# Optimization experiments

Hardware: AMD Instinct MI355X
Metric: run time of the kernel (lower is better)

The kernel has to match this reference:

```python
import jax, jax.numpy as jnp
import numpy as np

D = 768          # hidden_size
M = 8            # num_patchmerges
B = 16
S = 2048         # non-CLF tokens


def setup_inputs() -> dict:
    key = jax.random.key(0)
    ks = jax.random.split(key, 12)
    std = 0.02
    tokens = jax.random.normal(ks[0], (B, 1 + S, D), dtype=jnp.float32)
    lengths = jnp.maximum(jax.random.randint(ks[1], (B,), 0, S), 1).astype(jnp.int64)
    # PatchMerger: learned queries + layernorm params
    q = jax.random.normal(ks[2], (M, D), dtype=jnp.float32) * std
    ln_scale = jnp.ones((D,), dtype=jnp.float32)
    ln_bias = jnp.zeros((D,), dtype=jnp.float32)
    # mlp1: Linear(3D, D) -> GELU -> Linear(D, D)
    w1a = jax.random.normal(ks[3], (3 * D, D), dtype=jnp.float32) * std
    b1a = jnp.zeros((D,), dtype=jnp.float32)
    w2a = jax.random.normal(ks[4], (D, D), dtype=jnp.float32) * std
    b2a = jnp.zeros((D,), dtype=jnp.float32)
    # mlp2: Linear((1+M)D, D) -> GELU -> Linear(D, D)
    w1b = jax.random.normal(ks[5], ((1 + M) * D, D), dtype=jnp.float32) * std
    b1b = jnp.zeros((D,), dtype=jnp.float32)
    w2b = jax.random.normal(ks[6], (D, D), dtype=jnp.float32) * std
    b2b = jnp.zeros((D,), dtype=jnp.float32)
    return dict(tokens=tokens, lengths=lengths, q=q, ln_scale=ln_scale,
                ln_bias=ln_bias, w1a=w1a, b1a=b1a, w2a=w2a, b2a=b2a,
                w1b=w1b, b1b=b1b, w2b=w2b, b2b=b2b)


def _hpmlp(x, w1, b1, w2, b2):
    h = jax.nn.gelu(x @ w1 + b1, approximate=False)  # dropout=0 -> identity
    return h @ w2 + b2


def _layernorm(x, scale, bias, eps=1e-5):
    mu = jnp.mean(x, axis=-1, keepdims=True)
    var = jnp.var(x, axis=-1, keepdims=True)
    return (x - mu) * jax.lax.rsqrt(var + eps) * scale + bias


def reference(tokens, lengths, q, ln_scale, ln_bias,
              w1a, b1a, w2a, b2a, w1b, b1b, w2b, b2b):
    clf = tokens[:, 0]            # [B, D]
    x = tokens[:, 1:]             # [B, S, D]
    mask = jnp.arange(S)[None, :] < lengths[:, None]   # [B, S]
    mf = mask[..., None].astype(x.dtype)

    # fixed path: masked mean / max / min over valid tokens
    denom = lengths.astype(x.dtype)[:, None]
    mean_p = jnp.sum(x * mf, axis=1) / denom
    max_p = jnp.max(jnp.where(mask[..., None], x, -jnp.inf), axis=1)
    min_p = jnp.min(jnp.where(mask[..., None], x, jnp.inf), axis=1)
    pooled_trad = jnp.concatenate([mean_p, max_p, min_p], axis=-1)  # [B, 3D]
    out_fixed = _hpmlp(pooled_trad, w1a, b1a, w2a, b2a)

    # learned path: PatchMerger (masked attention from M learned queries)
    xn = _layernorm(x, ln_scale, ln_bias)
    scores = jnp.einsum('md,bsd->bms', q, xn) / jnp.sqrt(jnp.asarray(D, x.dtype))
    scores = jnp.where(mask[:, None, :], scores, -jnp.inf)
    attn = jax.nn.softmax(scores, axis=-1)                # [B, M, S]
    merged = jnp.einsum('bms,bsd->bmd', attn, x)          # [B, M, D]
    pooled_learn = jnp.concatenate([merged.reshape(B, M * D), clf], axis=-1)
    out_learn = _hpmlp(pooled_learn, w1b, b1b, w2b, b2b)

    return jnp.concatenate([out_fixed, out_learn], axis=-1)  # [B, 2D]
```

## Files before the change

### kernel.cpp

```cpp
#include <hip/hip_runtime.h>
#include <math.h>

#define SD 768
#define SB 16
#define SM 8
#define SS 2048
#define TOK_ROW 2049
#define NEG_INF (-__builtin_inff())

#define OFF_PPOOL   0
#define OFF_PO      2359296
#define OFF_PML     8650752
#define OFF_PTRAD   8667136
#define OFF_PLEARN  8704000
#define OFF_P1A     8814592
#define OFF_P1B     9035776
#define OFF_HA      9699328
#define OFF_HB      9711616
#define OFF_P2A     9723904
#define OFF_P2B     9797632

__device__ __forceinline__ int clen(int v) { return v < 1 ? 1 : (v > SS ? SS : v); }

__global__ __launch_bounds__(256, 2) void k1_flash(
    const float* __restrict__ tokens, const int* __restrict__ lengths,
    const float* __restrict__ q, const float* __restrict__ lns,
    const float* __restrict__ lnb, float* __restrict__ ppool,
    float* __restrict__ pO, float* __restrict__ pml) {
  int c = blockIdx.x, b = blockIdx.y;
  int len = clen(lengths[b]);
  int c0 = c * 32;
  if (c0 >= len) return;
  int tid = threadIdx.x, w = tid >> 6, lane = tid & 63;
  int mm = lane & 7;

  __shared__ float p_lds[4][8][8];
  __shared__ float pool_lds[4][3][SD];
  __shared__ float O_lds[SM][SD];
  __shared__ float l_lds[4][8];

  if (tid < 256) { (&p_lds[0][0][0])[tid] = 0.f; }

  float4 qr[8][3];
  float qs1sel, qbsel;
  {
    float4 l4[3], lb4[3];
    #pragma unroll
    for (int g = 0; g < 3; ++g) {
      l4[g] = *(const float4*)(lns + g * 256 + lane * 4);
      lb4[g] = *(const float4*)(lnb + g * 256 + lane * 4);
    }
    float qs1r[8], qbr[8];
    #pragma unroll
    for (int m = 0; m < 8; ++m) {
      float s1 = 0.f, sb = 0.f;
      #pragma unroll
      for (int g = 0; g < 3; ++g) {
        float4 qv = *(const float4*)(q + m * SD + g * 256 + lane * 4);
        float4 qs;
        qs.x = qv.x * l4[g].x; qs.y = qv.y * l4[g].y;
        qs.z = qv.z * l4[g].z; qs.w = qv.w * l4[g].w;
        qr[m][g] = qs;
        s1 += qs.x + qs.y + qs.z + qs.w;
        sb += qv.x * lb4[g].x + qv.y * lb4[g].y + qv.z * lb4[g].z + qv.w * lb4[g].w;
      }
      #pragma unroll
      for (int o = 32; o; o >>= 1) { s1 += __shfl_xor(s1, o, 64); sb += __shfl_xor(sb, o, 64); }
      qs1r[m] = s1; qbr[m] = sb;
    }
    qs1sel = qs1r[0]; qbsel = qbr[0];
    #pragma unroll
    for (int m = 1; m < 8; ++m) {
      qs1sel = (mm == m) ? qs1r[m] : qs1sel;
      qbsel = (mm == m) ? qbr[m] : qbsel;
    }
  }
  __syncthreads();

  float psum[12], pmax[12], pmin[12];
  #pragma unroll
  for (int j = 0; j < 12; ++j) { psum[j] = 0.f; pmax[j] = NEG_INF; pmin[j] = -NEG_INF; }

  int srow = c0 + w * 8;
  int smax = len - srow; if (smax > 8) smax = 8; if (smax < 0) smax = 0;
  const float* xrow = tokens + ((size_t)b * TOK_ROW + 1 + srow) * SD;
  float l_run = 0.f;

  float4 nx0 = {}, nx1 = {}, nx2 = {};
  if (smax > 0) {
    nx0 = *(const float4*)(xrow + lane * 4);
    nx1 = *(const float4*)(xrow + 256 + lane * 4);
    nx2 = *(const float4*)(xrow + 512 + lane * 4);
  }
  for (int i = 0; i < smax; ++i) {
    float4 x0 = nx0, x1 = nx1, x2 = nx2;
    if (i + 1 < smax) {
      const float* xq = xrow + (size_t)(i + 1) * SD;
      nx0 = *(const float4*)(xq + lane * 4);
      nx1 = *(const float4*)(xq + 256 + lane * 4);
      nx2 = *(const float4*)(xq + 512 + lane * 4);
    }
    float xv[12] = {x0.x, x0.y, x0.z, x0.w, x1.x, x1.y, x1.z, x1.w,
                    x2.x, x2.y, x2.z, x2.w};
    float s1 = 0.f, s2 = 0.f;
    #pragma unroll
    for (int j = 0; j < 12; ++j) {
      float v = xv[j];
      psum[j] += v;
      pmax[j] = fmaxf(pmax[j], v);
      pmin[j] = fminf(pmin[j], v);
      s1 += v;
      s2 += v * v;
    }
    float d[8];
    #pragma unroll
    for (int m = 0; m < 8; ++m) {
      float4 a0 = qr[m][0], a1 = qr[m][1], a2 = qr[m][2];
      d[m] = a0.x * xv[0] + a0.y * xv[1] + a0.z * xv[2] + a0.w * xv[3]
           + a1.x * xv[4] + a1.y * xv[5] + a1.z * xv[6] + a1.w * xv[7]
           + a2.x * xv[8] + a2.y * xv[9] + a2.z * xv[10] + a2.w * xv[11];
    }
    #pragma unroll
    for (int o = 1; o <= 4; o <<= 1)
      #pragma unroll
      for (int m = 0; m < 8; ++m) d[m] += __shfl_xor(d[m], o, 64);
    float u = d[0];
    #pragma unroll
    for (int m = 1; m < 8; ++m) u = (mm == m) ? d[m] : u;
    #pragma unroll
    for (int o = 8; o <= 32; o <<= 1) {
      u += __shfl_xor(u, o, 64);
      s1 += __shfl_xor(s1, o, 64);
      s2 += __shfl_xor(s2, o, 64);
    }
    #pragma unroll
    for (int o = 1; o <= 4; o <<= 1) { s1 += __shfl_xor(s1, o, 64); s2 += __shfl_xor(s2, o, 64); }
    float mu = s1 * (1.f / 768.f);
    float var = s2 * (1.f / 768.f) - mu * mu;
    float rstd = rsqrtf(var + 1e-5f);
    float sc = (rstd * u - rstd * mu * qs1sel + qbsel) * 0.03608439182435161f;
    float pe = __expf(sc);
    l_run += pe;
    if (lane < 8) p_lds[w][i][lane] = pe;
  }

  #pragma unroll
  for (int g = 0; g < 3; ++g) {
    int dd = g * 256 + lane * 4;
    *(float4*)&pool_lds[w][0][dd] = make_float4(psum[g*4], psum[g*4+1], psum[g*4+2], psum[g*4+3]);
    *(float4*)&pool_lds[w][1][dd] = make_float4(pmax[g*4], pmax[g*4+1], pmax[g*4+2], pmax[g*4+3]);
    *(float4*)&pool_lds[w][2][dd] = make_float4(pmin[g*4], pmin[g*4+1], pmin[g*4+2], pmin[g*4+3]);
  }
  if (lane < 8) l_lds[w][lane] = l_run;
  __syncthreads();

  if (tid < 8) {
    size_t base = (size_t)(c * SB + b) * 16;
    pml[base + tid] = 0.f;
    pml[base + 8 + tid] = l_lds[0][tid] + l_lds[1][tid] + l_lds[2][tid] + l_lds[3][tid];
  }

  float O[8][12];
  #pragma unroll
  for (int m = 0; m < 8; ++m)
    #pragma unroll
    for (int j = 0; j < 12; ++j) O[m][j] = 0.f;
  float4 a0v = {}, a1v = {}, a2v = {}, b0v = {}, b1v = {}, b2v = {};
  if (smax > 0) {
    a0v = *(const float4*)(xrow + lane * 4);
    a1v = *(const float4*)(xrow + 256 + lane * 4);
    a2v = *(const float4*)(xrow + 512 + lane * 4);
  }
  if (smax > 1) {
    const float* xq = xrow + SD;
    b0v = *(const float4*)(xq + lane * 4);
    b1v = *(const float4*)(xq + 256 + lane * 4);
    b2v = *(const float4*)(xq + 512 + lane * 4);
  }
  for (int i = 0; i < smax; ++i) {
    float4 x0 = a0v, x1 = a1v, x2 = a2v;
    a0v = b0v; a1v = b1v; a2v = b2v;
    if (i + 2 < smax) {
      const float* xq = xrow + (size_t)(i + 2) * SD;
      b0v = *(const float4*)(xq + lane * 4);
      b1v = *(const float4*)(xq + 256 + lane * 4);
      b2v = *(const float4*)(xq + 512 + lane * 4);
    }
    float xv[12] = {x0.x, x0.y, x0.z, x0.w, x1.x, x1.y, x1.z, x1.w,
                    x2.x, x2.y, x2.z, x2.w};
    const float4* pr = (const float4*)&p_lds[w][i][0];
    float4 pa = pr[0], pb = pr[1];
    float pm[8] = {pa.x, pa.y, pa.z, pa.w, pb.x, pb.y, pb.z, pb.w};
    #pragma unroll
    for (int m = 0; m < 8; ++m)
      #pragma unroll
      for (int j = 0; j < 12; ++j) O[m][j] += pm[m] * xv[j];
  }
  #pragma unroll
  for (int r = 0; r < 4; ++r) {
    if (w == r) {
      #pragma unroll
      for (int m = 0; m < 8; ++m)
        #pragma unroll
        for (int g = 0; g < 3; ++g) {
          int dd = g * 256 + lane * 4;
          float4 mine = make_float4(O[m][g*4], O[m][g*4+1], O[m][g*4+2], O[m][g*4+3]);
          if (r == 0) {
            *(float4*)&O_lds[m][dd] = mine;
          } else {
            float4 cur = *(float4*)&O_lds[m][dd];
            cur.x += mine.x; cur.y += mine.y; cur.z += mine.z; cur.w += mine.w;
            *(float4*)&O_lds[m][dd] = cur;
          }
        }
    }
    __syncthreads();
  }

  size_t obase = (size_t)(c * SB + b) * 6144;
  const float* of = &O_lds[0][0];
  for (int j = tid * 4; j < 6144; j += 1024)
    *(float4*)&pO[obase + j] = *(const float4*)&of[j];

  size_t pbase = (size_t)(c * SB + b) * 2304;
  for (int j4 = tid * 4; j4 < 2304; j4 += 1024) {
    int stat = j4 / SD, dd = j4 - stat * SD;
    float4 v0 = *(float4*)&pool_lds[0][stat][dd];
    float4 v1 = *(float4*)&pool_lds[1][stat][dd];
    float4 v2 = *(float4*)&pool_lds[2][stat][dd];
    float4 v3 = *(float4*)&pool_lds[3][stat][dd];
    float4 r;
    if (stat == 0) {
      r.x = v0.x + v1.x + v2.x + v3.x; r.y = v0.y + v1.y + v2.y + v3.y;
      r.z = v0.z + v1.z + v2.z + v3.z; r.w = v0.w + v1.w + v2.w + v3.w;
    } else if (stat == 1) {
      r.x = fmaxf(fmaxf(v0.x, v1.x), fmaxf(v2.x, v3.x));
      r.y = fmaxf(fmaxf(v0.y, v1.y), fmaxf(v2.y, v3.y));
      r.z = fmaxf(fmaxf(v0.z, v1.z), fmaxf(v2.z, v3.z));
      r.w = fmaxf(fmaxf(v0.w, v1.w), fmaxf(v2.w, v3.w));
    } else {
      r.x = fminf(fminf(v0.x, v1.x), fminf(v2.x, v3.x));
      r.y = fminf(fminf(v0.y, v1.y), fminf(v2.y, v3.y));
      r.z = fminf(fminf(v0.z, v1.z), fminf(v2.z, v3.z));
      r.w = fminf(fminf(v0.w, v1.w), fminf(v2.w, v3.w));
    }
    *(float4*)&ppool[pbase + j4] = r;
  }
}

__global__ void k_combine(const float* __restrict__ ppool, const float* __restrict__ pO,
                          const float* __restrict__ pml, const float* __restrict__ tokens,
                          const int* __restrict__ lengths,
                          float* __restrict__ ptrad, float* __restrict__ plearn) {
  int tile = blockIdx.x, b = blockIdx.y;
  int len = clen(lengths[b]);
  int nv = (len + 31) >> 5;
  int tid = threadIdx.x;
  __shared__ float pml_lds[64][16];
  __shared__ float e_lds[64][8];
  __shared__ float Linv_lds[8];
  for (int t = tid; t < nv * 16; t += 256) {
    int cc = t >> 4, j = t & 15;
    pml_lds[cc][j] = pml[(size_t)(cc * SB + b) * 16 + j];
  }
  __syncthreads();
  if (tid < 8) {
    float M = NEG_INF;
    for (int cc = 0; cc < nv; ++cc) M = fmaxf(M, pml_lds[cc][tid]);
    float L = 0.f;
    for (int cc = 0; cc < nv; ++cc) {
      float e = __expf(pml_lds[cc][tid] - M);
      e_lds[cc][tid] = e;
      L += e * pml_lds[cc][8 + tid];
    }
    Linv_lds[tid] = 1.f / L;
  }
  __syncthreads();
  #pragma unroll
  for (int k = 0; k < 4; ++k) {
    int jj = tile * 1024 + k * 256 + tid;
    if (jj < 2304) {
      int stat = jj / SD;
      const float* pp = ppool + jj + (size_t)b * 2304;
      if (stat == 0) {
        float a0 = 0.f, a1 = 0.f, a2 = 0.f, a3 = 0.f;
        int cc = 0;
        for (; cc + 4 <= nv; cc += 4) {
          a0 += pp[(size_t)(cc    ) * SB * 2304];
          a1 += pp[(size_t)(cc + 1) * SB * 2304];
          a2 += pp[(size_t)(cc + 2) * SB * 2304];
          a3 += pp[(size_t)(cc + 3) * SB * 2304];
        }
        for (; cc < nv; ++cc) a0 += pp[(size_t)cc * SB * 2304];
        ptrad[b * 2304 + jj] = ((a0 + a1) + (a2 + a3)) / (float)len;
      } else if (stat == 1) {
        float a0 = NEG_INF, a1 = NEG_INF, a2 = NEG_INF, a3 = NEG_INF;
        int cc = 0;
        for (; cc + 4 <= nv; cc += 4) {
          a0 = fmaxf(a0, pp[(size_t)(cc    ) * SB * 2304]);
          a1 = fmaxf(a1, pp[(size_t)(cc + 1) * SB * 2304]);
          a2 = fmaxf(a2, pp[(size_t)(cc + 2) * SB * 2304]);
          a3 = fmaxf(a3, pp[(size_t)(cc + 3) * SB * 2304]);
        }
        for (; cc < nv; ++cc) a0 = fmaxf(a0, pp[(size_t)cc * SB * 2304]);
        ptrad[b * 2304 + jj] = fmaxf(fmaxf(a0, a1), fmaxf(a2, a3));
      } else {
        float a0 = -NEG_INF, a1 = -NEG_INF, a2 = -NEG_INF, a3 = -NEG_INF;
        int cc = 0;
        for (; cc + 4 <= nv; cc += 4) {
          a0 = fminf(a0, pp[(size_t)(cc    ) * SB * 2304]);
          a1 = fminf(a1, pp[(size_t)(cc + 1) * SB * 2304]);
          a2 = fminf(a2, pp[(size_t)(cc + 2) * SB * 2304]);
          a3 = fminf(a3, pp[(size_t)(cc + 3) * SB * 2304]);
        }
        for (; cc < nv; ++cc) a0 = fminf(a0, pp[(size_t)cc * SB * 2304]);
        ptrad[b * 2304 + jj] = fminf(fminf(a0, a1), fminf(a2, a3));
      }
    } else if (jj < 8448) {
      int t = jj - 2304;
      int m = t / SD;
      const float* po = pO + t + (size_t)b * 6144;
      float a0 = 0.f, a1 = 0.f, a2 = 0.f, a3 = 0.f;
      float a4 = 0.f, a5 = 0.f, a6 = 0.f, a7 = 0.f;
      int cc = 0;
      for (; cc + 8 <= nv; cc += 8) {
        a0 += po[(size_t)(cc    ) * SB * 6144] * e_lds[cc    ][m];
        a1 += po[(size_t)(cc + 1) * SB * 6144] * e_lds[cc + 1][m];
        a2 += po[(size_t)(cc + 2) * SB * 6144] * e_lds[cc + 2][m];
        a3 += po[(size_t)(cc + 3) * SB * 6144] * e_lds[cc + 3][m];
        a4 += po[(size_t)(cc + 4) * SB * 6144] * e_lds[cc + 4][m];
        a5 += po[(size_t)(cc + 5) * SB * 6144] * e_lds[cc + 5][m];
        a6 += po[(size_t)(cc + 6) * SB * 6144] * e_lds[cc + 6][m];
        a7 += po[(size_t)(cc + 7) * SB * 6144] * e_lds[cc + 7][m];
      }
      for (; cc < nv; ++cc) a0 += po[(size_t)cc * SB * 6144] * e_lds[cc][m];
      plearn[b * 6912 + t] = (((a0 + a1) + (a2 + a3)) + ((a4 + a5) + (a6 + a7))) * Linv_lds[m];
    } else {
      int dd = jj - 8448;
      plearn[b * 6912 + 6144 + dd] = tokens[(size_t)b * TOK_ROW * SD + dd];
    }
  }
}

__global__ __launch_bounds__(256) void gemm_partial(
    const float* __restrict__ XA, const float* __restrict__ WA, int ktA, float* __restrict__ PA,
    const float* __restrict__ XB, const float* __restrict__ WB, float* __restrict__ PB) {
  int nt = blockIdx.x, ky = blockIdx.y;
  const float *X, *W; float* P; int kt, ktN;
  if (ky < ktA) { X = XA; W = WA; P = PA; kt = ky; ktN = ktA; }
  else { X = XB; W = WB; P = PB; kt = ky - ktA; ktN = gridDim.y - ktA; }
  int K = ktN * 128;
  int k0 = kt * 128;
  __shared__ __align__(16) float xt[128 * 20];
  __shared__ float red[4][64][17];
  int tid = threadIdx.x;
  int kk = tid & 127, half = tid >> 7;
  #pragma unroll
  for (int u = 0; u < 8; ++u) {
    int b2 = half * 8 + u;
    xt[kk * 20 + b2] = X[b2 * K + k0 + kk];
  }
  __syncthreads();
  int w = tid >> 6, lane = tid & 63;
  int n = nt * 64 + lane;
  float acc[16];
  #pragma unroll
  for (int b2 = 0; b2 < 16; ++b2) acc[b2] = 0.f;
  const float* Wp = W + (size_t)k0 * SD + n;
  #pragma unroll 8
  for (int kj = 0; kj < 32; ++kj) {
    int k = w + kj * 4;
    float wv = Wp[(size_t)k * SD];
    const float4* xr = reinterpret_cast<const float4*>(xt + k * 20);
    float4 a0 = xr[0], a1 = xr[1], a2 = xr[2], a3 = xr[3];
    acc[0] += wv * a0.x; acc[1] += wv * a0.y; acc[2] += wv * a0.z; acc[3] += wv * a0.w;
    acc[4] += wv * a1.x; acc[5] += wv * a1.y; acc[6] += wv * a1.z; acc[7] += wv * a1.w;
    acc[8] += wv * a2.x; acc[9] += wv * a2.y; acc[10] += wv * a2.z; acc[11] += wv * a2.w;
    acc[12] += wv * a3.x; acc[13] += wv * a3.y; acc[14] += wv * a3.z; acc[15] += wv * a3.w;
  }
  #pragma unroll
  for (int b2 = 0; b2 < 16; ++b2) red[w][lane][b2] = acc[b2];
  __syncthreads();
  for (int i = tid; i < 1024; i += 256) {
    int nn = i & 63, b2 = i >> 6;
    float r = red[0][nn][b2] + red[1][nn][b2] + red[2][nn][b2] + red[3][nn][b2];
    P[(size_t)(kt * 16 + b2) * SD + nt * 64 + nn] = r;
  }
}

__global__ void gelu_reduce(const float* __restrict__ PA, const float* __restrict__ b1a,
                            float* __restrict__ HA, const float* __restrict__ PB,
                            const float* __restrict__ b1b, float* __restrict__ HB) {
  int y = blockIdx.y;
  int j = blockIdx.x * 256 + threadIdx.x;
  float r;
  if (y == 0) {
    r = b1a[j % SD];
    #pragma unroll
    for (int kt = 0; kt < 18; ++kt) r += PA[kt * 12288 + j];
    HA[j] = r * 0.5f * (1.f + erff(r * 0.70710678118654752f));
  } else {
    r = b1b[j % SD];
    #pragma unroll
    for (int kt = 0; kt < 54; ++kt) r += PB[kt * 12288 + j];
    HB[j] = r * 0.5f * (1.f + erff(r * 0.70710678118654752f));
  }
}

__global__ void final_reduce(const float* __restrict__ P2A, const float* __restrict__ b2a,
                             const float* __restrict__ P2B, const float* __restrict__ b2b,
                             float* __restrict__ out) {
  int y = blockIdx.y;
  const float* P = y ? P2B : P2A;
  const float* bias = y ? b2b : b2a;
  int j = blockIdx.x * 256 + threadIdx.x;
  float r = bias[j % SD];
  #pragma unroll
  for (int kt = 0; kt < 6; ++kt) r += P[kt * 12288 + j];
  int b = j / SD, nn = j - b * SD;
  out[b * 1536 + y * SD + nn] = r;
}

extern "C" void kernel_launch(void* const* d_in, const int* in_sizes, int n_in,
                              void* d_out, int out_size, void* d_ws, size_t ws_size,
                              hipStream_t stream) {
  const float* tokens = (const float*)d_in[0];
  const int* lengths  = (const int*)d_in[1];
  const float* q      = (const float*)d_in[2];
  const float* lns    = (const float*)d_in[3];
  const float* lnb    = (const float*)d_in[4];
  const float* w1a    = (const float*)d_in[5];
  const float* b1a    = (const float*)d_in[6];
  const float* w2a    = (const float*)d_in[7];
  const float* b2a    = (const float*)d_in[8];
  const float* w1b    = (const float*)d_in[9];
  const float* b1b    = (const float*)d_in[10];
  const float* w2b    = (const float*)d_in[11];
  const float* b2b    = (const float*)d_in[12];
  float* ws  = (float*)d_ws;
  float* out = (float*)d_out;

  float* ppool  = ws + OFF_PPOOL;
  float* pO     = ws + OFF_PO;
  float* pml    = ws + OFF_PML;
  float* ptrad  = ws + OFF_PTRAD;
  float* plearn = ws + OFF_PLEARN;
  float* p1a    = ws + OFF_P1A;
  float* p1b    = ws + OFF_P1B;
  float* ha     = ws + OFF_HA;
  float* hb     = ws + OFF_HB;
  float* p2a    = ws + OFF_P2A;
  float* p2b    = ws + OFF_P2B;

  k1_flash<<<dim3(64, 16), 256, 0, stream>>>(tokens, lengths, q, lns, lnb, ppool, pO, pml);
  k_combine<<<dim3(9, 16), 256, 0, stream>>>(ppool, pO, pml, tokens, lengths, ptrad, plearn);
  gemm_partial<<<dim3(12, 72), 256, 0, stream>>>(ptrad, w1a, 18, p1a, plearn, w1b, p1b);
  gelu_reduce<<<dim3(48, 2), 256, 0, stream>>>(p1a, b1a, ha, p1b, b1b, hb);
  gemm_partial<<<dim3(12, 12), 256, 0, stream>>>(ha, w2a, 6, p2a, hb, w2b, p2b);
  final_reduce<<<dim3(48, 2), 256, 0, stream>>>(p2a, b2a, p2b, b2b, out);
}
```

Before: 247.3 us.

## Replace partial-buffer combine kernels with atomic accumulation and fused normalization

```diff
diff --git a/kernel.cpp b/kernel.cpp
--- a/kernel.cpp
+++ b/kernel.cpp
@@ -8,38 +8,60 @@
 #define TOK_ROW 2049
 #define NEG_INF (-__builtin_inff())
 
-#define OFF_PPOOL   0
-#define OFF_PO      2359296
-#define OFF_PML     8650752
-#define OFF_PTRAD   8667136
-#define OFF_PLEARN  8704000
-#define OFF_P1A     8814592
-#define OFF_P1B     9035776
-#define OFF_HA      9699328
-#define OFF_HB      9711616
-#define OFF_P2A     9723904
-#define OFF_P2B     9797632
+#define OFF_PTRADS  0
+#define OFF_PLEARN  36864
+#define OFF_LTOT    147456
+#define OFF_P1A     147584
+#define OFF_P1B     368768
+#define OFF_HA      1032320
+#define OFF_HB      1044608
 
 __device__ __forceinline__ int clen(int v) { return v < 1 ? 1 : (v > SS ? SS : v); }
+
+__device__ __forceinline__ unsigned fenc(float f) {
+  unsigned u = __float_as_uint(f);
+  return (u & 0x80000000u) ? ~u : (u ^ 0x80000000u);
+}
+__device__ __forceinline__ float fdec(unsigned u) {
+  unsigned i = (u & 0x80000000u) ? (u ^ 0x80000000u) : ~u;
+  return __uint_as_float(i);
+}
+
+__global__ void k_init(float* __restrict__ ws, float* __restrict__ out,
+                       const float* __restrict__ b2a, const float* __restrict__ b2b) {
+  int i = blockIdx.x * 256 + threadIdx.x;
+  int stride = gridDim.x * 256;
+  for (int t = i; t < 147584; t += stride) {
+    unsigned v = (t >= 24576 && t < 36864) ? 0xFFFFFFFFu : 0u;
+    ((unsigned*)ws)[t] = v;
+  }
+  for (int t = i; t < 24576; t += stride) {
+    int b = t / 1536, r = t - b * 1536;
+    out[t] = (r < 768) ? b2a[r] : b2b[r - 768];
+  }
+}
 
 __global__ __launch_bounds__(256, 2) void k1_flash(
     const float* __restrict__ tokens, const int* __restrict__ lengths,
     const float* __restrict__ q, const float* __restrict__ lns,
-    const float* __restrict__ lnb, float* __restrict__ ppool,
-    float* __restrict__ pO, float* __restrict__ pml) {
+    const float* __restrict__ lnb, float* __restrict__ ptradS,
+    float* __restrict__ plearn, float* __restrict__ ltot) {
   int c = blockIdx.x, b = blockIdx.y;
   int len = clen(lengths[b]);
-  int c0 = c * 32;
+  int c0 = c * 64;
   if (c0 >= len) return;
   int tid = threadIdx.x, w = tid >> 6, lane = tid & 63;
   int mm = lane & 7;
 
-  __shared__ float p_lds[4][8][8];
+  __shared__ float p_lds[4][16][8];
   __shared__ float pool_lds[4][3][SD];
   __shared__ float O_lds[SM][SD];
   __shared__ float l_lds[4][8];
 
-  if (tid < 256) { (&p_lds[0][0][0])[tid] = 0.f; }
+  {
+    float* pf = &p_lds[0][0][0];
+    for (int i = tid; i < 512; i += 256) pf[i] = 0.f;
+  }
 
   float4 qr[8][3];
   float qs1sel, qbsel;
@@ -81,8 +103,8 @@
   #pragma unroll
   for (int j = 0; j < 12; ++j) { psum[j] = 0.f; pmax[j] = NEG_INF; pmin[j] = -NEG_INF; }
 
-  int srow = c0 + w * 8;
-  int smax = len - srow; if (smax > 8) smax = 8; if (smax < 0) smax = 0;
+  int srow = c0 + w * 16;
+  int smax = len - srow; if (smax > 16) smax = 16; if (smax < 0) smax = 0;
   const float* xrow = tokens + ((size_t)b * TOK_ROW + 1 + srow) * SD;
   float l_run = 0.f;
 
@@ -154,11 +176,9 @@
   if (lane < 8) l_lds[w][lane] = l_run;
   __syncthreads();
 
-  if (tid < 8) {
-    size_t base = (size_t)(c * SB + b) * 16;
-    pml[base + tid] = 0.f;
-    pml[base + 8 + tid] = l_lds[0][tid] + l_lds[1][tid] + l_lds[2][tid] + l_lds[3][tid];
-  }
+  if (tid < 8)
+    atomicAdd(&ltot[b * 8 + tid],
+              l_lds[0][tid] + l_lds[1][tid] + l_lds[2][tid] + l_lds[3][tid]);
 
   float O[8][12];
   #pragma unroll
@@ -217,138 +237,35 @@
     __syncthreads();
   }
 
-  size_t obase = (size_t)(c * SB + b) * 6144;
-  const float* of = &O_lds[0][0];
-  for (int j = tid * 4; j < 6144; j += 1024)
-    *(float4*)&pO[obase + j] = *(const float4*)&of[j];
-
-  size_t pbase = (size_t)(c * SB + b) * 2304;
-  for (int j4 = tid * 4; j4 < 2304; j4 += 1024) {
-    int stat = j4 / SD, dd = j4 - stat * SD;
-    float4 v0 = *(float4*)&pool_lds[0][stat][dd];
-    float4 v1 = *(float4*)&pool_lds[1][stat][dd];
-    float4 v2 = *(float4*)&pool_lds[2][stat][dd];
-    float4 v3 = *(float4*)&pool_lds[3][stat][dd];
-    float4 r;
-    if (stat == 0) {
-      r.x = v0.x + v1.x + v2.x + v3.x; r.y = v0.y + v1.y + v2.y + v3.y;
-      r.z = v0.z + v1.z + v2.z + v3.z; r.w = v0.w + v1.w + v2.w + v3.w;
-    } else if (stat == 1) {
-      r.x = fmaxf(fmaxf(v0.x, v1.x), fmaxf(v2.x, v3.x));
-      r.y = fmaxf(fmaxf(v0.y, v1.y), fmaxf(v2.y, v3.y));
-      r.z = fmaxf(fmaxf(v0.z, v1.z), fmaxf(v2.z, v3.z));
-      r.w = fmaxf(fmaxf(v0.w, v1.w), fmaxf(v2.w, v3.w));
-    } else {
-      r.x = fminf(fminf(v0.x, v1.x), fminf(v2.x, v3.x));
-      r.y = fminf(fminf(v0.y, v1.y), fminf(v2.y, v3.y));
-      r.z = fminf(fminf(v0.z, v1.z), fminf(v2.z, v3.z));
-      r.w = fminf(fminf(v0.w, v1.w), fminf(v2.w, v3.w));
-    }
-    *(float4*)&ppool[pbase + j4] = r;
-  }
-}
-
-__global__ void k_combine(const float* __restrict__ ppool, const float* __restrict__ pO,
-                          const float* __restrict__ pml, const float* __restrict__ tokens,
-                          const int* __restrict__ lengths,
-                          float* __restrict__ ptrad, float* __restrict__ plearn) {
-  int tile = blockIdx.x, b = blockIdx.y;
-  int len = clen(lengths[b]);
-  int nv = (len + 31) >> 5;
-  int tid = threadIdx.x;
-  __shared__ float pml_lds[64][16];
-  __shared__ float e_lds[64][8];
-  __shared__ float Linv_lds[8];
-  for (int t = tid; t < nv * 16; t += 256) {
-    int cc = t >> 4, j = t & 15;
-    pml_lds[cc][j] = pml[(size_t)(cc * SB + b) * 16 + j];
-  }
-  __syncthreads();
-  if (tid < 8) {
-    float M = NEG_INF;
-    for (int cc = 0; cc < nv; ++cc) M = fmaxf(M, pml_lds[cc][tid]);
-    float L = 0.f;
-    for (int cc = 0; cc < nv; ++cc) {
-      float e = __expf(pml_lds[cc][tid] - M);
-      e_lds[cc][tid] = e;
-      L += e * pml_lds[cc][8 + tid];
-    }
-    Linv_lds[tid] = 1.f / L;
-  }
-  __syncthreads();
-  #pragma unroll
-  for (int k = 0; k < 4; ++k) {
-    int jj = tile * 1024 + k * 256 + tid;
-    if (jj < 2304) {
-      int stat = jj / SD;
-      const float* pp = ppool + jj + (size_t)b * 2304;
-      if (stat == 0) {
-        float a0 = 0.f, a1 = 0.f, a2 = 0.f, a3 = 0.f;
-        int cc = 0;
-        for (; cc + 4 <= nv; cc += 4) {
-          a0 += pp[(size_t)(cc    ) * SB * 2304];
-          a1 += pp[(size_t)(cc + 1) * SB * 2304];
-          a2 += pp[(size_t)(cc + 2) * SB * 2304];
-          a3 += pp[(size_t)(cc + 3) * SB * 2304];
-        }
-        for (; cc < nv; ++cc) a0 += pp[(size_t)cc * SB * 2304];
-        ptrad[b * 2304 + jj] = ((a0 + a1) + (a2 + a3)) / (float)len;
-      } else if (stat == 1) {
-        float a0 = NEG_INF, a1 = NEG_INF, a2 = NEG_INF, a3 = NEG_INF;
-        int cc = 0;
-        for (; cc + 4 <= nv; cc += 4) {
-          a0 = fmaxf(a0, pp[(size_t)(cc    ) * SB * 2304]);
-          a1 = fmaxf(a1, pp[(size_t)(cc + 1) * SB * 2304]);
-          a2 = fmaxf(a2, pp[(size_t)(cc + 2) * SB * 2304]);
-          a3 = fmaxf(a3, pp[(size_t)(cc + 3) * SB * 2304]);
-        }
-        for (; cc < nv; ++cc) a0 = fmaxf(a0, pp[(size_t)cc * SB * 2304]);
-        ptrad[b * 2304 + jj] = fmaxf(fmaxf(a0, a1), fmaxf(a2, a3));
-      } else {
-        float a0 = -NEG_INF, a1 = -NEG_INF, a2 = -NEG_INF, a3 = -NEG_INF;
-        int cc = 0;
-        for (; cc + 4 <= nv; cc += 4) {
-          a0 = fminf(a0, pp[(size_t)(cc    ) * SB * 2304]);
-          a1 = fminf(a1, pp[(size_t)(cc + 1) * SB * 2304]);
-          a2 = fminf(a2, pp[(size_t)(cc + 2) * SB * 2304]);
-          a3 = fminf(a3, pp[(size_t)(cc + 3) * SB * 2304]);
-        }
-        for (; cc < nv; ++cc) a0 = fminf(a0, pp[(size_t)cc * SB * 2304]);
-        ptrad[b * 2304 + jj] = fminf(fminf(a0, a1), fminf(a2, a3));
-      }
-    } else if (jj < 8448) {
-      int t = jj - 2304;
-      int m = t / SD;
-      const float* po = pO + t + (size_t)b * 6144;
-      float a0 = 0.f, a1 = 0.f, a2 = 0.f, a3 = 0.f;
-      float a4 = 0.f, a5 = 0.f, a6 = 0.f, a7 = 0.f;
-      int cc = 0;
-      for (; cc + 8 <= nv; cc += 8) {
-        a0 += po[(size_t)(cc    ) * SB * 6144] * e_lds[cc    ][m];
-        a1 += po[(size_t)(cc + 1) * SB * 6144] * e_lds[cc + 1][m];
-        a2 += po[(size_t)(cc + 2) * SB * 6144] * e_lds[cc + 2][m];
-        a3 += po[(size_t)(cc + 3) * SB * 6144] * e_lds[cc + 3][m];
-        a4 += po[(size_t)(cc + 4) * SB * 6144] * e_lds[cc + 4][m];
-        a5 += po[(size_t)(cc + 5) * SB * 6144] * e_lds[cc + 5][m];
-        a6 += po[(size_t)(cc + 6) * SB * 6144] * e_lds[cc + 6][m];
-        a7 += po[(size_t)(cc + 7) * SB * 6144] * e_lds[cc + 7][m];
-      }
-      for (; cc < nv; ++cc) a0 += po[(size_t)cc * SB * 6144] * e_lds[cc][m];
-      plearn[b * 6912 + t] = (((a0 + a1) + (a2 + a3)) + ((a4 + a5) + (a6 + a7))) * Linv_lds[m];
-    } else {
-      int dd = jj - 8448;
-      plearn[b * 6912 + 6144 + dd] = tokens[(size_t)b * TOK_ROW * SD + dd];
-    }
-  }
+  {
+    const float* of = &O_lds[0][0];
+    for (int j = tid; j < 6144; j += 256)
+      atomicAdd(&plearn[(size_t)b * 6912 + j], of[j]);
+  }
+  for (int j = tid; j < 768; j += 256) {
+    float s = pool_lds[0][0][j] + pool_lds[1][0][j] + pool_lds[2][0][j] + pool_lds[3][0][j];
+    atomicAdd(&ptradS[b * 768 + j], s);
+    float mx = fmaxf(fmaxf(pool_lds[0][1][j], pool_lds[1][1][j]),
+                     fmaxf(pool_lds[2][1][j], pool_lds[3][1][j]));
+    atomicMax((unsigned*)&ptradS[12288 + b * 768 + j], fenc(mx));
+    float mn = fminf(fminf(pool_lds[0][2][j], pool_lds[1][2][j]),
+                     fminf(pool_lds[2][2][j], pool_lds[3][2][j]));
+    atomicMin((unsigned*)&ptradS[24576 + b * 768 + j], fenc(mn));
+  }
+  if (c == 0)
+    for (int dd = tid; dd < 768; dd += 256)
+      plearn[(size_t)b * 6912 + 6144 + dd] = tokens[(size_t)b * TOK_ROW * SD + dd];
 }
 
 __global__ __launch_bounds__(256) void gemm_partial(
     const float* __restrict__ XA, const float* __restrict__ WA, int ktA, float* __restrict__ PA,
-    const float* __restrict__ XB, const float* __restrict__ WB, float* __restrict__ PB) {
+    const float* __restrict__ XB, const float* __restrict__ WB, float* __restrict__ PB,
+    const int* __restrict__ lengths, const float* __restrict__ ltot,
+    int modeA, int modeB, int epi) {
   int nt = blockIdx.x, ky = blockIdx.y;
-  const float *X, *W; float* P; int kt, ktN;
-  if (ky < ktA) { X = XA; W = WA; P = PA; kt = ky; ktN = ktA; }
-  else { X = XB; W = WB; P = PB; kt = ky - ktA; ktN = gridDim.y - ktA; }
+  const float *X, *W; float* P; int kt, ktN, mode;
+  if (ky < ktA) { X = XA; W = WA; P = PA; kt = ky; ktN = ktA; mode = modeA; }
+  else { X = XB; W = WB; P = PB; kt = ky - ktA; ktN = gridDim.y - ktA; mode = modeB; }
   int K = ktN * 128;
   int k0 = kt * 128;
   __shared__ __align__(16) float xt[128 * 20];
@@ -358,7 +275,19 @@
   #pragma unroll
   for (int u = 0; u < 8; ++u) {
     int b2 = half * 8 + u;
-    xt[kk * 20 + b2] = X[b2 * K + k0 + kk];
+    float f;
+    if (mode == 0) {
+      int s = kt / 6;
+      f = X[s * 12288 + b2 * 768 + (k0 - s * 768) + kk];
+      if (s == 0) f = f / (float)clen(lengths[b2]);
+      else        f = fdec(__float_as_uint(f));
+    } else if (mode == 1) {
+      f = X[b2 * 6912 + k0 + kk];
+      if (kt < 48) f = f / ltot[b2 * 8 + (k0 / 768)];
+    } else {
+      f = X[b2 * K + k0 + kk];
+    }
+    xt[kk * 20 + b2] = f;
   }
   __syncthreads();
   int w = tid >> 6, lane = tid & 63;
@@ -384,7 +313,8 @@
   for (int i = tid; i < 1024; i += 256) {
     int nn = i & 63, b2 = i >> 6;
     float r = red[0][nn][b2] + red[1][nn][b2] + red[2][nn][b2] + red[3][nn][b2];
-    P[(size_t)(kt * 16 + b2) * SD + nt * 64 + nn] = r;
+    if (epi == 0) P[(size_t)(kt * 16 + b2) * SD + nt * 64 + nn] = r;
+    else          atomicAdd(&P[b2 * 1536 + nt * 64 + nn], r);
   }
 }
 
@@ -405,20 +335,6 @@
     for (int kt = 0; kt < 54; ++kt) r += PB[kt * 12288 + j];
     HB[j] = r * 0.5f * (1.f + erff(r * 0.70710678118654752f));
   }
-}
-
-__global__ void final_reduce(const float* __restrict__ P2A, const float* __restrict__ b2a,
-                             const float* __restrict__ P2B, const float* __restrict__ b2b,
-                             float* __restrict__ out) {
-  int y = blockIdx.y;
-  const float* P = y ? P2B : P2A;
-  const float* bias = y ? b2b : b2a;
-  int j = blockIdx.x * 256 + threadIdx.x;
-  float r = bias[j % SD];
-  #pragma unroll
-  for (int kt = 0; kt < 6; ++kt) r += P[kt * 12288 + j];
-  int b = j / SD, nn = j - b * SD;
-  out[b * 1536 + y * SD + nn] = r;
 }
 
 extern "C" void kernel_launch(void* const* d_in, const int* in_sizes, int n_in,
@@ -440,22 +356,22 @@
   float* ws  = (float*)d_ws;
   float* out = (float*)d_out;
 
-  float* ppool  = ws + OFF_PPOOL;
-  float* pO     = ws + OFF_PO;
-  float* pml    = ws + OFF_PML;
-  float* ptrad  = ws + OFF_PTRAD;
+  float* ptradS = ws + OFF_PTRADS;
   float* plearn = ws + OFF_PLEARN;
+  float* ltot   = ws + OFF_LTOT;
   float* p1a    = ws + OFF_P1A;
   float* p1b    = ws + OFF_P1B;
   float* ha     = ws + OFF_HA;
   float* hb     = ws + OFF_HB;
-  float* p2a    = ws + OFF_P2A;
-  float* p2b    = ws + OFF_P2B;
-
-  k1_flash<<<dim3(64, 16), 256, 0, stream>>>(tokens, lengths, q, lns, lnb, ppool, pO, pml);
-  k_combine<<<dim3(9, 16), 256, 0, stream>>>(ppool, pO, pml, tokens, lengths, ptrad, plearn);
-  gemm_partial<<<dim3(12, 72), 256, 0, stream>>>(ptrad, w1a, 18, p1a, plearn, w1b, p1b);
+
+  k_init<<<dim3(128), 256, 0, stream>>>(ws, out, b2a, b2b);
+  k1_flash<<<dim3(32, 16), 256, 0, stream>>>(tokens, lengths, q, lns, lnb,
+                                             ptradS, plearn, ltot);
+  gemm_partial<<<dim3(12, 72), 256, 0, stream>>>(ptradS, w1a, 18, p1a,
+                                                 plearn, w1b, p1b,
+                                                 lengths, ltot, 0, 1, 0);
   gelu_reduce<<<dim3(48, 2), 256, 0, stream>>>(p1a, b1a, ha, p1b, b1b, hb);
-  gemm_partial<<<dim3(12, 12), 256, 0, stream>>>(ha, w2a, 6, p2a, hb, w2b, p2b);
-  final_reduce<<<dim3(48, 2), 256, 0, stream>>>(p2a, b2a, p2b, b2b, out);
-}
+  gemm_partial<<<dim3(12, 12), 256, 0, stream>>>(ha, w2a, 6, out,
+                                                 hb, w2b, out + 768,
+                                                 lengths, ltot, 2, 2, 1);
+}
```

Result: faster. 219.1 us (-11.4%).
